# Optimization experiments

Hardware: AMD Instinct MI355X
Metric: run time of the kernel (lower is better)

Reference implementation:

```python
import jax, jax.numpy as jnp
import numpy as np

N = 8       # number of mesh faces (the module's global n)
KC_K = 4    # kernel-correlation points per channel
K_CLS = 40  # output classes


def _lin(x, W, b):
    return x @ W + b


def setup_inputs() -> dict:
    key = jax.random.key(0)
    ks = iter(jax.random.split(key, 64))
    def w(shape, s=0.02):
        return jax.random.normal(next(ks), shape, jnp.float32) * s
    inp = {
        "center": jax.random.normal(next(ks), (N * 3,), jnp.float32),
        "corner": jax.random.normal(next(ks), (N * 9,), jnp.float32),
        "normal": jax.random.normal(next(ks), (N * 3,), jnp.float32),
        "neighbour": jax.random.randint(next(ks), (N * 3,), 0, N),
        # spatial_Des (flattened GEMVs)
        "sp_W1": w((N * 3, N * 64)), "sp_b1": w((N * 64,)),
        "sp_W2": w((N * 64, N * 64)), "sp_b2": w((N * 64,)),
        # Face_Rotate_Conv: conv1d(1,32,6) == dense (6->32) at single position
        "frc_Wc": w((32, 6)), "frc_bc": w((32,)),
        "frc_W3": w((32, 64)), "frc_b3": w((64,)),
        "frc_W4": w((64, 64)), "frc_b4": w((64,)),
        # Kernel_Correlation learnable kernel (64, k, 3)
        "kc_kernel": w((64, KC_K, 3), 1.0),
        # structural_Des per-face linears (131 -> 131)
        "st_W1": w((131, 131)), "st_b1": w((131,)),
        "st_W2": w((131, 131)), "st_b2": w((131,)),
        # Mesh1: Combination1 / Aggregation1
        "c1_W1": w((N * 195, N * 200)), "c1_b1": w((N * 200,)),
        "c1_W2": w((N * 200, N * 256)), "c1_b2": w((N * 256,)),
        "a1_W3": w((N * 131, N * 512)), "a1_b3": w((N * 512,)),
        "a1_W4": w((N * 512, N * 256)), "a1_b4": w((N * 256,)),
        # Mesh2: Combination2 / Aggregation2
        "c2_W1": w((N * 512, N * 512)), "c2_b1": w((N * 512,)),
        "c2_W2": w((N * 512, N * 512)), "c2_b2": w((N * 512,)),
        "a2_W3": w((N * 256, N * 512)), "a2_b3": w((N * 512,)),
        "a2_W4": w((N * 512, N * 512)), "a2_b4": w((N * 512,)),
        # Net per-face 1024 linears
        "nt_W1": w((1024, 1024)), "nt_b1": w((1024,)),
        "nt_W2": w((1024, 1024)), "nt_b2": w((1024,)),
        # mlp2 (flattened)
        "m2_W1": w((N * 1792, N * 1024)), "m2_b1": w((N * 1024,)),
        "m2_W2": w((N * 1024, N * 1024)), "m2_b2": w((N * 1024,)),
        # mlp3 classifier head
        "m3_W1": w((1024, 512)), "m3_b1": w((512,)),
        "m3_W2": w((512, 256)), "m3_b2": w((256,)),
        "m3_W3": w((256, K_CLS)), "m3_b3": w((K_CLS,)),
    }
    return inp


def _forward(center, corner, normal, nb,
             sp_W1, sp_b1, sp_W2, sp_b2,
             frc_Wc, frc_bc, frc_W3, frc_b3, frc_W4, frc_b4,
             kc_kernel, st_W1, st_b1, st_W2, st_b2,
             c1_W1, c1_b1, c1_W2, c1_b2, a1_W3, a1_b3, a1_W4, a1_b4,
             c2_W1, c2_b1, c2_W2, c2_b2, a2_W3, a2_b3, a2_W4, a2_b4,
             nt_W1, nt_b1, nt_W2, nt_b2,
             m2_W1, m2_b1, m2_W2, m2_b2,
             m3_W1, m3_b1, m3_W2, m3_b2, m3_W3, m3_b3):
    relu = jax.nn.relu
    # spatial descriptor (flattened GEMV over n*3 -> n*64 -> n*64)
    y = _lin(relu(_lin(center, sp_W1, sp_b1)), sp_W2, sp_b2)  # (N*64,)
    # Face_Rotate_Conv: per-face corner pairs -> conv(6->32) -> mean -> MLP
    c = corner.reshape(N, 3, 3)
    pairs = jnp.stack([
        jnp.concatenate([c[:, 0], c[:, 1]], axis=-1),
        jnp.concatenate([c[:, 1], c[:, 2]], axis=-1),
        jnp.concatenate([c[:, 2], c[:, 0]], axis=-1)], axis=1)  # (N,3,6)
    conv = pairs @ frc_Wc.T + frc_bc                            # (N,3,32)
    frc = _lin(relu(_lin(conv.mean(axis=1), frc_W3, frc_b3)), frc_W4, frc_b4)  # (N,64)
    # Kernel_Correlation: (1/(4k)) * sum_l exp(-||n_i - K[m,l]||^2) / (2*sigma^2), sigma=1
    nr = normal.reshape(N, 3)
    diff = nr[:, None, None, :] - kc_kernel[None]               # (N,64,k,3)
    kc = (jnp.exp(-jnp.sum(diff * diff, axis=-1)) / 2.0).sum(axis=-1) / (KC_K * 4)  # (N,64)
    # structural descriptor: per-face [normal(3) | kc(64) | frc(64)] = 131 -> 131 -> 131
    feat = jnp.concatenate([nr, kc, frc], axis=-1)              # (N,131)
    z = _lin(relu(_lin(feat, st_W1, st_b1)), st_W2, st_b2)      # (N,131)
    z_flat = z.reshape(-1)
    # Mesh1
    out1 = _lin(relu(_lin(jnp.concatenate([y, z_flat]), c1_W1, c1_b1)), c1_W2, c1_b2)  # (N*256,)
    agg1 = ((z + z[nb].sum(axis=1)) / 4.0).reshape(-1)          # mean of self + 3 neighbours
    out2 = _lin(relu(_lin(agg1, a1_W3, a1_b3)), a1_W4, a1_b4)   # (N*256,)
    # Mesh2
    out3 = _lin(relu(_lin(jnp.concatenate([out1, out2]), c2_W1, c2_b1)), c2_W2, c2_b2)  # (N*512,)
    o2 = out2.reshape(N, 256)
    agg2 = ((o2 + o2[nb].sum(axis=1)) / 4.0).reshape(-1)
    out4 = _lin(relu(_lin(agg2, a2_W3, a2_b3)), a2_W4, a2_b4)   # (N*512,)
    # head
    out5 = jnp.concatenate([out3, out4]).reshape(N, 1024)
    out5 = _lin(relu(_lin(out5, nt_W1, nt_b1)), nt_W2, nt_b2).reshape(-1)  # (N*1024,)
    out6 = jnp.concatenate([out5, out3, out1])                  # (N*1792,)
    h = _lin(relu(_lin(out6, m2_W1, m2_b1)), m2_W2, m2_b2).reshape(N, 1024)
    g = h.max(axis=0)                                           # global max-pool over faces
    logits = _lin(relu(_lin(relu(_lin(g, m3_W1, m3_b1)), m3_W2, m3_b2)), m3_W3, m3_b3)
    return logits  # (K_CLS,)


def reference(center, corner, normal, neighbour,
              sp_W1, sp_b1, sp_W2, sp_b2,
              frc_Wc, frc_bc, frc_W3, frc_b3, frc_W4, frc_b4,
              kc_kernel, st_W1, st_b1, st_W2, st_b2,
              c1_W1, c1_b1, c1_W2, c1_b2, a1_W3, a1_b3, a1_W4, a1_b4,
              c2_W1, c2_b1, c2_W2, c2_b2, a2_W3, a2_b3, a2_W4, a2_b4,
              nt_W1, nt_b1, nt_W2, nt_b2,
              m2_W1, m2_b1, m2_W2, m2_b2,
              m3_W1, m3_b1, m3_W2, m3_b2, m3_W3, m3_b3):
    nb = neighbour.reshape(N, 3)
    return _forward(center, corner, normal, nb,
                    sp_W1, sp_b1, sp_W2, sp_b2,
                    frc_Wc, frc_bc, frc_W3, frc_b3, frc_W4, frc_b4,
                    kc_kernel, st_W1, st_b1, st_W2, st_b2,
                    c1_W1, c1_b1, c1_W2, c1_b2, a1_W3, a1_b3, a1_W4, a1_b4,
                    c2_W1, c2_b1, c2_W2, c2_b2, a2_W3, a2_b3, a2_W4, a2_b4,
                    nt_W1, nt_b1, nt_W2, nt_b2,
                    m2_W1, m2_b1, m2_W2, m2_b2,
                    m3_W1, m3_b1, m3_W2, m3_b2, m3_W3, m3_b3)
```

## Files before the change

### kernel.cpp

```cpp
#include <hip/hip_runtime.h>
#include <cstdint>

#define TPB 256
typedef __attribute__((ext_vector_type(4))) float f4;


__global__ __launch_bounds__(TPB) void stage1_kernel(
    const float* __restrict__ center, const float* __restrict__ corner,
    const float* __restrict__ normal,
    const float* __restrict__ spW1, const float* __restrict__ spb1,
    const float* __restrict__ spW2, const float* __restrict__ spb2,
    const float* __restrict__ Wc, const float* __restrict__ bc,
    const float* __restrict__ W3, const float* __restrict__ b3,
    const float* __restrict__ W4, const float* __restrict__ b4,
    const float* __restrict__ kck,
    const float* __restrict__ stW1, const float* __restrict__ stb1,
    const float* __restrict__ stW2, const float* __restrict__ stb2,
    float* __restrict__ ws) {
    int tid = threadIdx.x;
    int b = blockIdx.x;
    if (b < 8) {
        int f = b;
        __shared__ float sc[9], sn[3], sm[32], shh[64], sf[131], sh2[131];
        if (tid < 9) sc[tid] = corner[f * 9 + tid];
        if (tid < 3) { sn[tid] = normal[f * 3 + tid]; sf[tid] = normal[f * 3 + tid]; }
        __syncthreads();
        if (tid < 32) {
            float acc = 0.f;
            for (int p = 0; p < 3; ++p) {
                const float* a  = &sc[3 * p];
                const float* b2 = &sc[3 * ((p + 1) % 3)];
                float d = bc[tid];
                for (int k = 0; k < 3; ++k)
                    d += a[k] * Wc[tid * 6 + k] + b2[k] * Wc[tid * 6 + 3 + k];
                acc += d;
            }
            sm[tid] = acc * (1.f / 3.f);
        }
        __syncthreads();
        if (tid < 64) {
            float h = b3[tid];
            for (int o = 0; o < 32; ++o) h = fmaf(sm[o], W3[o * 64 + tid], h);
            shh[tid] = fmaxf(h, 0.f);
        }
        if (tid < 64) {
            float s = 0.f;
            for (int l = 0; l < 4; ++l) {
                float dx = sn[0] - kck[(tid * 4 + l) * 3 + 0];
                float dy = sn[1] - kck[(tid * 4 + l) * 3 + 1];
                float dz = sn[2] - kck[(tid * 4 + l) * 3 + 2];
                s += expf(-(dx * dx + dy * dy + dz * dz));
            }
            sf[3 + tid] = s * (1.f / 32.f);
        }
        __syncthreads();
        if (tid < 64) {
            float v = b4[tid];
            for (int k = 0; k < 64; ++k) v = fmaf(shh[k], W4[k * 64 + tid], v);
            sf[67 + tid] = v;
        }
        __syncthreads();
        if (tid < 131) {
            float a = stb1[tid];
            for (int k = 0; k < 131; ++k) a = fmaf(sf[k], stW1[k * 131 + tid], a);
            sh2[tid] = fmaxf(a, 0.f);
        }
        __syncthreads();
        if (tid < 131) {
            float a = stb2[tid];
            for (int k = 0; k < 131; ++k) a = fmaf(sh2[k], stW2[k * 131 + tid], a);
            ws[1024 + f * 131 + tid] = a;
        }
    } else if (b < 12) {
        int bs = b - 8;
        __shared__ float sctr[24], st1[512];
        if (tid < 24) sctr[tid] = center[tid];
        __syncthreads();
        for (int j = tid; j < 512; j += TPB) {
            float a = spb1[j];
            for (int i = 0; i < 24; ++i) a = fmaf(sctr[i], spW1[i * 512 + j], a);
            st1[j] = fmaxf(a, 0.f);
        }
        __syncthreads();
        if (tid < 128) {
            int j = bs * 128 + tid;
            float a = spb2[j];
            for (int k = 0; k < 512; ++k) a = fmaf(st1[k], spW2[k * 512 + j], a);
            ws[512 + j] = a;
        }
    } else {
        int zb = b - 12;
        f4 z4 = {0.f, 0.f, 0.f, 0.f};
        f4* p = (f4*)(ws + 2072);
        int n4 = (67928 - 2072) / 4;
        for (int i = zb * TPB + tid; i < n4; i += 32 * TPB) p[i] = z4;
    }
}

struct Desc {
    const float* x; const float* W; float* out; const float* bias;
    const int* nb;
    int in_dim, out_dim, chunk, ntile, nchunk, nvec, xs, os;
    int op;
    int aggdim;
    int nt;
    int nblocks;
};
struct Descs { Desc d[3]; int nd; };

__global__ __launch_bounds__(TPB) void mg_kernel(Descs D) {
    int bid = blockIdx.x;
    int di = 0;
    while (di + 1 < D.nd && bid >= D.d[di].nblocks) { bid -= D.d[di].nblocks; ++di; }
    Desc d = D.d[di];
    int tid = threadIdx.x;
    if (d.op == 4) {
        int i = bid * TPB + tid;
        int n4 = d.in_dim >> 2;
        if (i < n4) ((f4*)d.out)[i] = ((const f4*)d.x)[i];
        return;
    }
    __shared__ float sx[512];
    __shared__ float sval[512];
    __shared__ unsigned short sidx[512];
    __shared__ int segc[10];
    int per = d.ntile * d.nchunk;
    int vec = bid / per;
    int r = bid - vec * per;
    int ci = r / d.ntile;
    int tile = r - ci * d.ntile;
    const float* x = d.x + (size_t)vec * d.xs;
    float* out = d.out + (size_t)vec * d.os;
    int row0 = ci * d.chunk;
    int rows = min(d.chunk, d.in_dim - row0);
    for (int t = tid; t < rows; t += TPB) {
        int idx = row0 + t;
        float v;
        if (d.op == 2) {
            int i = idx / d.aggdim, k = idx - i * d.aggdim;
            const int* nb = d.nb + i * 3;
            v = 0.25f * (x[i * d.aggdim + k] + x[nb[0] * d.aggdim + k] +
                         x[nb[1] * d.aggdim + k] + x[nb[2] * d.aggdim + k]);
        } else if (d.op == 3) {
            v = x[idx];
#pragma unroll
            for (int f = 1; f < 8; ++f) v = fmaxf(v, x[f * d.in_dim + idx]);
        } else {
            v = x[idx];
            if (d.op == 1 || d.op == 5) v = fmaxf(v, 0.f);
        }
        sx[t] = v;
    }
    __syncthreads();

    if (d.op == 5) {
        int wave = tid >> 6, lane = tid & 63;
        int nseg = (rows + 63) >> 6;
        for (int s = wave; s < nseg; s += 4) {
            int t = s * 64 + lane;
            bool p = (t < rows) && (sx[t] > 0.f);
            unsigned long long m = __ballot(p);
            if (lane == 0) segc[s] = __popcll(m);
        }
        __syncthreads();
        if (tid == 0) {
            int acc = 0;
            for (int s = 0; s < nseg; ++s) { int c = segc[s]; segc[s] = acc; acc += c; }
            segc[nseg] = acc;
        }
        __syncthreads();
        for (int s = wave; s < nseg; s += 4) {
            int t = s * 64 + lane;
            bool p = (t < rows) && (sx[t] > 0.f);
            unsigned long long m = __ballot(p);
            int rk = __popcll(m & ((1ull << lane) - 1ull));
            if (p) {
                int o = segc[s] + rk;
                sval[o] = sx[t];
                sidx[o] = (unsigned short)t;
            }
        }
        __syncthreads();
        int cnt = segc[nseg];
        int j = tile * (TPB * 4) + tid * 4;
        if (j >= d.out_dim) return;
        const float* wb = d.W + j;
        float ax = 0.f, ay = 0.f, az = 0.f, aw = 0.f;
        if (d.nt) {
#pragma unroll 8
            for (int t = 0; t < cnt; ++t) {
                float xv = sval[t];
                f4 w = __builtin_nontemporal_load(
                    (const f4*)(wb + (size_t)(row0 + (int)sidx[t]) * d.out_dim));
                ax = fmaf(xv, w[0], ax); ay = fmaf(xv, w[1], ay);
                az = fmaf(xv, w[2], az); aw = fmaf(xv, w[3], aw);
            }
        } else {
#pragma unroll 8
            for (int t = 0; t < cnt; ++t) {
                float xv = sval[t];
                f4 w = *(const f4*)(wb + (size_t)(row0 + (int)sidx[t]) * d.out_dim);
                ax = fmaf(xv, w[0], ax); ay = fmaf(xv, w[1], ay);
                az = fmaf(xv, w[2], az); aw = fmaf(xv, w[3], aw);
            }
        }
        if (ci == 0 && d.bias) {
            ax += d.bias[j]; ay += d.bias[j + 1];
            az += d.bias[j + 2]; aw += d.bias[j + 3];
        }
        unsafeAtomicAdd(&out[j + 0], ax);
        unsafeAtomicAdd(&out[j + 1], ay);
        unsafeAtomicAdd(&out[j + 2], az);
        unsafeAtomicAdd(&out[j + 3], aw);
        return;
    }

    int j = tile * (TPB * 4) + tid * 4;
    if (j >= d.out_dim) return;
    const float* wp = d.W + (size_t)row0 * d.out_dim + j;
    float ax = 0.f, ay = 0.f, az = 0.f, aw = 0.f;
    if (d.nt) {
#pragma unroll 16
        for (int t = 0; t < rows; ++t) {
            f4 w = __builtin_nontemporal_load((const f4*)wp);
            float xv = sx[t];
            ax = fmaf(xv, w[0], ax); ay = fmaf(xv, w[1], ay);
            az = fmaf(xv, w[2], az); aw = fmaf(xv, w[3], aw);
            wp += d.out_dim;
        }
    } else {
#pragma unroll 16
        for (int t = 0; t < rows; ++t) {
            f4 w = *(const f4*)wp;
            float xv = sx[t];
            ax = fmaf(xv, w[0], ax); ay = fmaf(xv, w[1], ay);
            az = fmaf(xv, w[2], az); aw = fmaf(xv, w[3], aw);
            wp += d.out_dim;
        }
    }
    if (ci == 0 && d.bias) {
        ax += d.bias[j]; ay += d.bias[j + 1]; az += d.bias[j + 2]; aw += d.bias[j + 3];
    }
    unsafeAtomicAdd(&out[j + 0], ax);
    unsafeAtomicAdd(&out[j + 1], ay);
    unsafeAtomicAdd(&out[j + 2], az);
    unsafeAtomicAdd(&out[j + 3], aw);
}

__global__ __launch_bounds__(TPB) void tail_kernel(
    const float* __restrict__ m3h1, const float* __restrict__ W2,
    const float* __restrict__ b2, const float* __restrict__ W3,
    const float* __restrict__ b3, float* __restrict__ out) {
    __shared__ float s1[512], red[256];
    int tid = threadIdx.x, j = blockIdx.x;
    for (int k = tid; k < 512; k += TPB) s1[k] = fmaxf(m3h1[k], 0.f);
    __syncthreads();
    float a = b2[tid];
    for (int i = 0; i < 512; ++i) a = fmaf(s1[i], W2[i * 256 + tid], a);
    a = fmaxf(a, 0.f);
    red[tid] = a * W3[tid * 40 + j];
    __syncthreads();
    for (int s = 128; s > 0; s >>= 1) {
        if (tid < s) red[tid] += red[tid + s];
        __syncthreads();
    }
    if (tid == 0) out[j] = red[0] + b3[j];
}

static Desc gemv_desc(const float* x, const float* W, float* out, const float* bias,
                      int in, int outd, int chunk, int op,
                      int nvec = 1, int xs = 0, int os = 0,
                      const int* nb = nullptr, int aggdim = 0, int nt = 0) {
    Desc d{};
    d.x = x; d.W = W; d.out = out; d.bias = bias; d.nb = nb;
    d.in_dim = in; d.out_dim = outd; d.chunk = chunk;
    d.ntile = (outd + TPB * 4 - 1) / (TPB * 4);
    d.nchunk = (in + chunk - 1) / chunk;
    d.nvec = nvec; d.xs = xs; d.os = os;
    d.op = op; d.aggdim = aggdim; d.nt = nt;
    d.nblocks = d.ntile * d.nchunk * nvec;
    return d;
}
static Desc copy_desc(const float* src, float* dst, int n) {
    Desc d{};
    d.x = src; d.out = dst; d.in_dim = n; d.op = 4;
    d.nblocks = (n / 4 + TPB - 1) / TPB;
    return d;
}
static void mg1(hipStream_t s, Desc a) {
    Descs D{}; D.d[0] = a; D.nd = 1;
    mg_kernel<<<a.nblocks, TPB, 0, s>>>(D);
}
static void mg2(hipStream_t s, Desc a, Desc b) {
    Descs D{}; D.d[0] = a; D.d[1] = b; D.nd = 2;
    mg_kernel<<<a.nblocks + b.nblocks, TPB, 0, s>>>(D);
}
static void mg3(hipStream_t s, Desc a, Desc b, Desc c) {
    Descs D{}; D.d[0] = a; D.d[1] = b; D.d[2] = c; D.nd = 3;
    mg_kernel<<<a.nblocks + b.nblocks + c.nblocks, TPB, 0, s>>>(D);
}

extern "C" void kernel_launch(void* const* d_in, const int* in_sizes, int n_in,
                              void* d_out, int out_size, void* d_ws, size_t ws_size,
                              hipStream_t stream) {
    const float* center    = (const float*)d_in[0];
    const float* corner    = (const float*)d_in[1];
    const float* normal    = (const float*)d_in[2];
    const int*   neighbour = (const int*)  d_in[3];
    const float* sp_W1 = (const float*)d_in[4];
    const float* sp_b1 = (const float*)d_in[5];
    const float* sp_W2 = (const float*)d_in[6];
    const float* sp_b2 = (const float*)d_in[7];
    const float* frc_Wc = (const float*)d_in[8];
    const float* frc_bc = (const float*)d_in[9];
    const float* frc_W3 = (const float*)d_in[10];
    const float* frc_b3 = (const float*)d_in[11];
    const float* frc_W4 = (const float*)d_in[12];
    const float* frc_b4 = (const float*)d_in[13];
    const float* kc_kernel = (const float*)d_in[14];
    const float* st_W1 = (const float*)d_in[15];
    const float* st_b1 = (const float*)d_in[16];
    const float* st_W2 = (const float*)d_in[17];
    const float* st_b2 = (const float*)d_in[18];
    const float* c1_W1 = (const float*)d_in[19];
    const float* c1_b1 = (const float*)d_in[20];
    const float* c1_W2 = (const float*)d_in[21];
    const float* c1_b2 = (const float*)d_in[22];
    const float* a1_W3 = (const float*)d_in[23];
    const float* a1_b3 = (const float*)d_in[24];
    const float* a1_W4 = (const float*)d_in[25];
    const float* a1_b4 = (const float*)d_in[26];
    const float* c2_W1 = (const float*)d_in[27];
    const float* c2_b1 = (const float*)d_in[28];
    const float* c2_W2 = (const float*)d_in[29];
    const float* c2_b2 = (const float*)d_in[30];
    const float* a2_W3 = (const float*)d_in[31];
    const float* a2_b3 = (const float*)d_in[32];
    const float* a2_W4 = (const float*)d_in[33];
    const float* a2_b4 = (const float*)d_in[34];
    const float* nt_W1 = (const float*)d_in[35];
    const float* nt_b1 = (const float*)d_in[36];
    const float* nt_W2 = (const float*)d_in[37];
    const float* nt_b2 = (const float*)d_in[38];
    const float* m2_W1 = (const float*)d_in[39];
    const float* m2_b1 = (const float*)d_in[40];
    const float* m2_W2 = (const float*)d_in[41];
    const float* m2_b2 = (const float*)d_in[42];
    const float* m3_W1 = (const float*)d_in[43];
    const float* m3_b1 = (const float*)d_in[44];
    const float* m3_W2 = (const float*)d_in[45];
    const float* m3_b2 = (const float*)d_in[46];
    const float* m3_W3 = (const float*)d_in[47];
    const float* m3_b3 = (const float*)d_in[48];

    float* ws = (float*)d_ws;
    float* C1IN  = ws + 512;
    float* Z     = ws + 1024;
    float* C1H   = ws + 2072;
    float* OUT12 = ws + 3672;
    float* A1H   = ws + 7768;
    float* C2H   = ws + 11864;
    float* OUT34 = ws + 15960;
    float* A2H   = ws + 24152;
    float* NTH   = ws + 28248;
    float* OUT6  = ws + 36440;
    float* M2H   = ws + 50776;
    float* HBUF  = ws + 58968;
    float* M3H1  = ws + 67160;

    stage1_kernel<<<44, TPB, 0, stream>>>(center, corner, normal,
        sp_W1, sp_b1, sp_W2, sp_b2, frc_Wc, frc_bc, frc_W3, frc_b3,
        frc_W4, frc_b4, kc_kernel, st_W1, st_b1, st_W2, st_b2, ws);

    mg2(stream,
        gemv_desc(C1IN, c1_W1, C1H, c1_b1, 1560, 1600, 26, 0),
        gemv_desc(Z, a1_W3, A1H, a1_b3, 1048, 4096, 17, 2, 1, 0, 0, neighbour, 131));
    mg2(stream,
        gemv_desc(C1H, c1_W2, OUT12, c1_b2, 1600, 2048, 28, 5),
        gemv_desc(A1H, a1_W4, OUT12 + 2048, a1_b4, 4096, 2048, 64, 5));
    mg2(stream,
        gemv_desc(OUT12, c2_W1, C2H, c2_b1, 4096, 4096, 64, 0),
        gemv_desc(OUT12 + 2048, a2_W3, A2H, a2_b3, 2048, 4096, 32, 2, 1, 0, 0, neighbour, 256));
    mg3(stream,
        gemv_desc(C2H, c2_W2, OUT34, c2_b2, 4096, 4096, 64, 5),
        gemv_desc(A2H, a2_W4, OUT34 + 4096, a2_b4, 4096, 4096, 64, 5),
        copy_desc(OUT12, OUT6 + 12288, 2048));
    mg2(stream,
        gemv_desc(OUT34, nt_W1, NTH, nt_b1, 1024, 1024, 64, 0, 8, 1024, 1024),
        copy_desc(OUT34, OUT6 + 8192, 4096));
    mg1(stream,
        gemv_desc(NTH, nt_W2, OUT6, nt_b2, 1024, 1024, 64, 5, 8, 1024, 1024));
    mg1(stream, gemv_desc(OUT6, m2_W1, M2H, m2_b1, 14336, 8192, 448, 0,
                          1, 0, 0, nullptr, 0, 1));
    mg1(stream, gemv_desc(M2H, m2_W2, HBUF, m2_b2, 8192, 8192, 256, 5,
                          1, 0, 0, nullptr, 0, 1));
    mg1(stream, gemv_desc(HBUF, m3_W1, M3H1, m3_b1, 1024, 512, 16, 3));
    tail_kernel<<<40, TPB, 0, stream>>>(M3H1, m3_W2, m3_b2, m3_W3, m3_b3,
                                        (float*)d_out);
}
```

Baseline: 267.6 us.

## Fuse Net per-face MLP and classifier head into dedicated kernels, drop launches

```diff
diff --git a/kernel.cpp b/kernel.cpp
--- a/kernel.cpp
+++ b/kernel.cpp
@@ -247,18 +247,78 @@
     unsafeAtomicAdd(&out[j + 3], aw);
 }
 
-__global__ __launch_bounds__(TPB) void tail_kernel(
-    const float* __restrict__ m3h1, const float* __restrict__ W2,
-    const float* __restrict__ b2, const float* __restrict__ W3,
-    const float* __restrict__ b3, float* __restrict__ out) {
-    __shared__ float s1[512], red[256];
+__global__ __launch_bounds__(TPB) void ntf_kernel(
+    const float* __restrict__ OUT34, const float* __restrict__ OUT12,
+    const float* __restrict__ W1, const float* __restrict__ b1,
+    const float* __restrict__ W2, const float* __restrict__ b2,
+    float* __restrict__ OUT6) {
+    int b = blockIdx.x, tid = threadIdx.x;
+    if (b >= 8) {
+        if (b < 12) {
+            int i = (b - 8) * TPB + tid;
+            ((f4*)(OUT6 + 8192))[i] = ((const f4*)OUT34)[i];
+        } else {
+            int i = (b - 12) * TPB + tid;
+            ((f4*)(OUT6 + 12288))[i] = ((const f4*)OUT12)[i];
+        }
+        return;
+    }
+    __shared__ float sx[1024], sh[1024];
+    for (int k = tid; k < 1024; k += TPB) sx[k] = OUT34[b * 1024 + k];
+    __syncthreads();
+    int j = tid * 4;
+    float a0 = b1[j], a1 = b1[j + 1], a2 = b1[j + 2], a3 = b1[j + 3];
+#pragma unroll 16
+    for (int k = 0; k < 1024; ++k) {
+        f4 w = *(const f4*)(W1 + (size_t)k * 1024 + j);
+        float xv = sx[k];
+        a0 = fmaf(xv, w[0], a0); a1 = fmaf(xv, w[1], a1);
+        a2 = fmaf(xv, w[2], a2); a3 = fmaf(xv, w[3], a3);
+    }
+    sh[j] = fmaxf(a0, 0.f); sh[j + 1] = fmaxf(a1, 0.f);
+    sh[j + 2] = fmaxf(a2, 0.f); sh[j + 3] = fmaxf(a3, 0.f);
+    __syncthreads();
+    float c0 = b2[j], c1 = b2[j + 1], c2 = b2[j + 2], c3 = b2[j + 3];
+#pragma unroll 16
+    for (int k = 0; k < 1024; ++k) {
+        f4 w = *(const f4*)(W2 + (size_t)k * 1024 + j);
+        float xv = sh[k];
+        c0 = fmaf(xv, w[0], c0); c1 = fmaf(xv, w[1], c1);
+        c2 = fmaf(xv, w[2], c2); c3 = fmaf(xv, w[3], c3);
+    }
+    OUT6[b * 1024 + j] = c0;     OUT6[b * 1024 + j + 1] = c1;
+    OUT6[b * 1024 + j + 2] = c2; OUT6[b * 1024 + j + 3] = c3;
+}
+
+__global__ __launch_bounds__(TPB) void tail2_kernel(
+    const float* __restrict__ hbuf,
+    const float* __restrict__ W1, const float* __restrict__ b1,
+    const float* __restrict__ W2, const float* __restrict__ b2,
+    const float* __restrict__ W3, const float* __restrict__ b3,
+    float* __restrict__ out) {
+    __shared__ float g[1024], h1[512], red[256];
     int tid = threadIdx.x, j = blockIdx.x;
-    for (int k = tid; k < 512; k += TPB) s1[k] = fmaxf(m3h1[k], 0.f);
-    __syncthreads();
-    float a = b2[tid];
-    for (int i = 0; i < 512; ++i) a = fmaf(s1[i], W2[i * 256 + tid], a);
-    a = fmaxf(a, 0.f);
-    red[tid] = a * W3[tid * 40 + j];
+    for (int k = tid; k < 1024; k += TPB) {
+        float m = hbuf[k];
+#pragma unroll
+        for (int f = 1; f < 8; ++f) m = fmaxf(m, hbuf[f * 1024 + k]);
+        g[k] = m;
+    }
+    __syncthreads();
+    float a0 = b1[tid], a1 = b1[tid + 256];
+#pragma unroll 8
+    for (int k = 0; k < 1024; ++k) {
+        float xv = g[k];
+        a0 = fmaf(xv, W1[(size_t)k * 512 + tid], a0);
+        a1 = fmaf(xv, W1[(size_t)k * 512 + tid + 256], a1);
+    }
+    h1[tid] = fmaxf(a0, 0.f); h1[tid + 256] = fmaxf(a1, 0.f);
+    __syncthreads();
+    float c0 = b2[tid];
+#pragma unroll 8
+    for (int k = 0; k < 512; ++k) c0 = fmaf(h1[k], W2[k * 256 + tid], c0);
+    c0 = fmaxf(c0, 0.f);
+    red[tid] = c0 * W3[tid * 40 + j];
     __syncthreads();
     for (int s = 128; s > 0; s >>= 1) {
         if (tid < s) red[tid] += red[tid + s];
@@ -281,12 +341,6 @@
     d.nblocks = d.ntile * d.nchunk * nvec;
     return d;
 }
-static Desc copy_desc(const float* src, float* dst, int n) {
-    Desc d{};
-    d.x = src; d.out = dst; d.in_dim = n; d.op = 4;
-    d.nblocks = (n / 4 + TPB - 1) / TPB;
-    return d;
-}
 static void mg1(hipStream_t s, Desc a) {
     Descs D{}; D.d[0] = a; D.nd = 1;
     mg_kernel<<<a.nblocks, TPB, 0, s>>>(D);
@@ -294,10 +348,6 @@
 static void mg2(hipStream_t s, Desc a, Desc b) {
     Descs D{}; D.d[0] = a; D.d[1] = b; D.nd = 2;
     mg_kernel<<<a.nblocks + b.nblocks, TPB, 0, s>>>(D);
-}
-static void mg3(hipStream_t s, Desc a, Desc b, Desc c) {
-    Descs D{}; D.d[0] = a; D.d[1] = b; D.d[2] = c; D.nd = 3;
-    mg_kernel<<<a.nblocks + b.nblocks + c.nblocks, TPB, 0, s>>>(D);
 }
 
 extern "C" void kernel_launch(void* const* d_in, const int* in_sizes, int n_in,
@@ -362,39 +412,40 @@
     float* C2H   = ws + 11864;
     float* OUT34 = ws + 15960;
     float* A2H   = ws + 24152;
-    float* NTH   = ws + 28248;
     float* OUT6  = ws + 36440;
     float* M2H   = ws + 50776;
     float* HBUF  = ws + 58968;
-    float* M3H1  = ws + 67160;
 
     stage1_kernel<<<44, TPB, 0, stream>>>(center, corner, normal,
         sp_W1, sp_b1, sp_W2, sp_b2, frc_Wc, frc_bc, frc_W3, frc_b3,
         frc_W4, frc_b4, kc_kernel, st_W1, st_b1, st_W2, st_b2, ws);
 
     mg2(stream,
-        gemv_desc(C1IN, c1_W1, C1H, c1_b1, 1560, 1600, 26, 0),
-        gemv_desc(Z, a1_W3, A1H, a1_b3, 1048, 4096, 17, 2, 1, 0, 0, neighbour, 131));
+        gemv_desc(C1IN, c1_W1, C1H, c1_b1, 1560, 1600, 26, 0,
+                  1, 0, 0, nullptr, 0, 1),
+        gemv_desc(Z, a1_W3, A1H, a1_b3, 1048, 4096, 17, 2,
+                  1, 0, 0, neighbour, 131, 1));
     mg2(stream,
-        gemv_desc(C1H, c1_W2, OUT12, c1_b2, 1600, 2048, 28, 5),
-        gemv_desc(A1H, a1_W4, OUT12 + 2048, a1_b4, 4096, 2048, 64, 5));
+        gemv_desc(C1H, c1_W2, OUT12, c1_b2, 1600, 2048, 28, 5,
+                  1, 0, 0, nullptr, 0, 1),
+        gemv_desc(A1H, a1_W4, OUT12 + 2048, a1_b4, 4096, 2048, 64, 5,
+                  1, 0, 0, nullptr, 0, 1));
     mg2(stream,
-        gemv_desc(OUT12, c2_W1, C2H, c2_b1, 4096, 4096, 64, 0),
-        gemv_desc(OUT12 + 2048, a2_W3, A2H, a2_b3, 2048, 4096, 32, 2, 1, 0, 0, neighbour, 256));
-    mg3(stream,
-        gemv_desc(C2H, c2_W2, OUT34, c2_b2, 4096, 4096, 64, 5),
-        gemv_desc(A2H, a2_W4, OUT34 + 4096, a2_b4, 4096, 4096, 64, 5),
-        copy_desc(OUT12, OUT6 + 12288, 2048));
+        gemv_desc(OUT12, c2_W1, C2H, c2_b1, 4096, 4096, 64, 0,
+                  1, 0, 0, nullptr, 0, 1),
+        gemv_desc(OUT12 + 2048, a2_W3, A2H, a2_b3, 2048, 4096, 32, 2,
+                  1, 0, 0, neighbour, 256, 1));
     mg2(stream,
-        gemv_desc(OUT34, nt_W1, NTH, nt_b1, 1024, 1024, 64, 0, 8, 1024, 1024),
-        copy_desc(OUT34, OUT6 + 8192, 4096));
-    mg1(stream,
-        gemv_desc(NTH, nt_W2, OUT6, nt_b2, 1024, 1024, 64, 5, 8, 1024, 1024));
+        gemv_desc(C2H, c2_W2, OUT34, c2_b2, 4096, 4096, 64, 5,
+                  1, 0, 0, nullptr, 0, 1),
+        gemv_desc(A2H, a2_W4, OUT34 + 4096, a2_b4, 4096, 4096, 64, 5,
+                  1, 0, 0, nullptr, 0, 1));
+    ntf_kernel<<<14, TPB, 0, stream>>>(OUT34, OUT12, nt_W1, nt_b1,
+                                       nt_W2, nt_b2, OUT6);
     mg1(stream, gemv_desc(OUT6, m2_W1, M2H, m2_b1, 14336, 8192, 448, 0,
                           1, 0, 0, nullptr, 0, 1));
     mg1(stream, gemv_desc(M2H, m2_W2, HBUF, m2_b2, 8192, 8192, 256, 5,
                           1, 0, 0, nullptr, 0, 1));
-    mg1(stream, gemv_desc(HBUF, m3_W1, M3H1, m3_b1, 1024, 512, 16, 3));
-    tail_kernel<<<40, TPB, 0, stream>>>(M3H1, m3_W2, m3_b2, m3_W3, m3_b3,
-                                        (float*)d_out);
-}
+    tail2_kernel<<<40, TPB, 0, stream>>>(HBUF, m3_W1, m3_b1, m3_W2, m3_b2,
+                                         m3_W3, m3_b3, (float*)d_out);
+}
```

New measurement: 384.1 us. 1.44x slower.
